# Kernel optimization log

Hardware: AMD Instinct MI355X
Metric: run time of the kernel (lower is better)

The kernel has to match this reference:

```python
import jax, jax.numpy as jnp
import numpy as np

N = 200000      # nodes
E = 1600000     # edges
B = 1000        # graphs
SD = 64         # state_dim
AD = 32         # action_dim
H = 128         # HIDDEN_LAYER
EPS = 1e-5


def setup_inputs() -> dict:
    key = jax.random.key(0)
    ks = jax.random.split(key, 16)
    x = jax.random.normal(ks[0], (N, SD), dtype=jnp.float32)
    action = jax.random.normal(ks[1], (N, AD), dtype=jnp.float32)
    edge_index = jax.random.randint(ks[2], (2, E), 0, N, dtype=jnp.int64)
    batch_size = jnp.sort(jax.random.randint(ks[3], (N,), 0, B, dtype=jnp.int64))
    # parameters (Linear weights stored [in, out]; torch init std=0.1 for fc layers)
    W_gcn = jax.random.normal(ks[4], (SD, H), dtype=jnp.float32) / np.sqrt(SD)
    b_gcn = jnp.zeros((H,), jnp.float32)
    g0 = jnp.ones((H,), jnp.float32); be0 = jnp.zeros((H,), jnp.float32)
    W1 = jax.random.normal(ks[5], (H, H), dtype=jnp.float32) * 0.1
    b1 = jnp.zeros((H,), jnp.float32)
    g1 = jnp.ones((H,), jnp.float32); be1 = jnp.zeros((H,), jnp.float32)
    W2 = jax.random.normal(ks[6], (AD, H), dtype=jnp.float32) * 0.1
    b2 = jnp.zeros((H,), jnp.float32)
    g2 = jnp.ones((H,), jnp.float32); be2 = jnp.zeros((H,), jnp.float32)
    W3 = jax.random.normal(ks[7], (2 * H, 1), dtype=jnp.float32) * 0.1
    b3 = jnp.zeros((1,), jnp.float32)
    return dict(x=x, action=action, W_gcn=W_gcn, b_gcn=b_gcn, g0=g0, be0=be0,
                W1=W1, b1=b1, g1=g1, be1=be1, W2=W2, b2=b2, g2=g2, be2=be2,
                W3=W3, b3=b3, edge_index=edge_index, batch_size=batch_size)


def _bn(h, gamma, beta):
    # BatchNorm1d, training-mode batch statistics over the node axis
    mu = jnp.mean(h, axis=0)
    var = jnp.var(h, axis=0)
    return (h - mu) * jax.lax.rsqrt(var + EPS) * gamma + beta


def _gcn(x, edge_index, W, b):
    # GCN conv with self-loops and symmetric normalization:
    # out_i = sum_{j in N(i) u {i}} (d_i d_j)^{-1/2} (x_j W) + b
    loops = jnp.arange(N, dtype=edge_index.dtype)
    src = jnp.concatenate([edge_index[0], loops])
    dst = jnp.concatenate([edge_index[1], loops])
    deg = jax.ops.segment_sum(jnp.ones_like(dst, dtype=x.dtype), dst, num_segments=N)
    dinv = jax.lax.rsqrt(deg)                       # deg >= 1 due to self-loops
    norm = dinv[src] * dinv[dst]                    # [E+N]
    xw = x @ W                                      # [N, H]
    msg = xw[src] * norm[:, None]                   # [E+N, H]
    return jax.ops.segment_sum(msg, dst, num_segments=N) + b


def reference(x, action, W_gcn, b_gcn, g0, be0, W1, b1, g1, be1,
              W2, b2, g2, be2, W3, b3, edge_index, batch_size):
    h0 = jax.nn.relu(_gcn(x, edge_index, W_gcn, b_gcn))
    h0n = _bn(h0, g0, be0)
    h1 = jax.nn.relu(h0n @ W1 + b1)
    h1n = _bn(h1, g1, be1)
    h2 = jax.nn.relu(action @ W2 + b2)
    h2n = _bn(h2, g2, be2)
    feat = jnp.concatenate([h1n, h2n], axis=1)      # [N, 2H]
    sums = jax.ops.segment_sum(feat, batch_size, num_segments=B)
    cnts = jax.ops.segment_sum(jnp.ones((N,), feat.dtype), batch_size, num_segments=B)
    pooled = sums / jnp.maximum(cnts, 1.0)[:, None]  # [B, 2H]
    return pooled @ W3 + b3                          # [B, 1]
```

## Files before the change

### kernel.cpp

```cpp
#include <hip/hip_runtime.h>

typedef unsigned short u16;
typedef unsigned int   u32;
typedef __bf16 bf16x8 __attribute__((ext_vector_type(8)));
typedef float  f32x4  __attribute__((ext_vector_type(4)));

#define EPS 1e-5f
#define BSHIFT 9

__device__ __forceinline__ float b2f(u16 u){ union{u32 i; float f;} v; v.i=((u32)u)<<16; return v.f; }
__device__ __forceinline__ u16 f2b(float f){
  u32 x = __float_as_uint(f);
  u32 r = x + 0x7fffu + ((x>>16)&1u);
  return (u16)(r>>16);
}

template<int K, bool RELU, bool HASBIAS, bool AF32, bool POOL>
__global__ __launch_bounds__(256) void k_gemm(const void* __restrict__ Av,
                                              const u16* __restrict__ BhiT,
                                              const u16* __restrict__ BloT,
                                              const float* __restrict__ bias,
                                              u16* __restrict__ C,
                                              float* __restrict__ stats,
                                              const int* __restrict__ batch,
                                              float* __restrict__ P, int M)
{
  constexpr int KM = K / 8;
  constexpr int KR = K / 32;
  __shared__ u16 lds[2 * 64 * K];
  __shared__ float sred[64], qred[64];
  const int tid = threadIdx.x;
  const int halfg = gridDim.x >> 1;
  const int ch = (blockIdx.x >= halfg) ? 1 : 0;
  const int t0 = blockIdx.x - ch * halfg;
  for (int i = tid; i < 64 * KM; i += 256) {
    const int n = i / KM, kb = i % KM;
    const int kb2 = kb ^ (n & (KM - 1));
    const int gsrc = ((ch * 64 + n) * KM + kb) * 8;
    *(uint4*)(&lds[(n * KM + kb2) * 8])          = *(const uint4*)(BhiT + gsrc);
    *(uint4*)(&lds[64 * K + (n * KM + kb2) * 8]) = *(const uint4*)(BloT + gsrc);
  }
  if (tid < 64) { sred[tid] = 0.f; qred[tid] = 0.f; }
  __syncthreads();
  const int wid = tid >> 6, lane = tid & 63, q = lane >> 4, r16 = lane & 15;
  const int nmt = (M + 127) >> 7;
  float ls[4], lq[4];
#pragma unroll
  for (int nb = 0; nb < 4; nb++) { ls[nb] = 0.f; lq[nb] = 0.f; }
  float bv[4];
#pragma unroll
  for (int nb = 0; nb < 4; nb++) bv[nb] = HASBIAS ? bias[ch * 64 + nb * 16 + r16] : 0.f;

  for (int mt = t0; mt < nmt; mt += halfg) {
    const int row0 = mt << 7;
    const bool ok1 = (row0 + 64) < M;

    bf16x8 av[2][KR];
    if (AF32) {
      const float* Af = (const float*)Av + (size_t)(row0 + (wid << 4) + r16) * K + q * 8;
#pragma unroll
      for (int kk = 0; kk < KR; kk++) {
        f32x4 x0 = *(const f32x4*)(Af + kk * 32);
        f32x4 x1 = *(const f32x4*)(Af + kk * 32 + 4);
#pragma unroll
        for (int j = 0; j < 4; j++) { av[0][kk][j] = (__bf16)x0[j]; av[0][kk][4 + j] = (__bf16)x1[j]; }
      }
      if (ok1) {
        const float* Ag = Af + (size_t)64 * K;
#pragma unroll
        for (int kk = 0; kk < KR; kk++) {
          f32x4 x0 = *(const f32x4*)(Ag + kk * 32);
          f32x4 x1 = *(const f32x4*)(Ag + kk * 32 + 4);
#pragma unroll
          for (int j = 0; j < 4; j++) { av[1][kk][j] = (__bf16)x0[j]; av[1][kk][4 + j] = (__bf16)x1[j]; }
        }
      }
    } else {
      const u16* Ab = (const u16*)Av + (size_t)(row0 + (wid << 4) + r16) * K + q * 8;
#pragma unroll
      for (int kk = 0; kk < KR; kk++) av[0][kk] = *(const bf16x8*)(Ab + kk * 32);
      if (ok1) {
#pragma unroll
        for (int kk = 0; kk < KR; kk++) av[1][kk] = *(const bf16x8*)(Ab + (size_t)64 * K + kk * 32);
      }
    }

    f32x4 acc[2][4];
#pragma unroll
    for (int rt = 0; rt < 2; rt++)
#pragma unroll
      for (int nb = 0; nb < 4; nb++) acc[rt][nb] = (f32x4){0.f, 0.f, 0.f, 0.f};
#pragma unroll
    for (int kk = 0; kk < KR; kk++) {
#pragma unroll
      for (int nb = 0; nb < 4; nb++) {
        const int n = nb * 16 + r16;
        const int kb2 = (kk * 4 + q) ^ (n & (KM - 1));
        const bf16x8 bh = *(const bf16x8*)(&lds[(n * KM + kb2) * 8]);
        const bf16x8 bl = *(const bf16x8*)(&lds[64 * K + (n * KM + kb2) * 8]);
        acc[0][nb] = __builtin_amdgcn_mfma_f32_16x16x32_bf16(av[0][kk], bh, acc[0][nb], 0, 0, 0);
        acc[0][nb] = __builtin_amdgcn_mfma_f32_16x16x32_bf16(av[0][kk], bl, acc[0][nb], 0, 0, 0);
        if (ok1) {
          acc[1][nb] = __builtin_amdgcn_mfma_f32_16x16x32_bf16(av[1][kk], bh, acc[1][nb], 0, 0, 0);
          acc[1][nb] = __builtin_amdgcn_mfma_f32_16x16x32_bf16(av[1][kk], bl, acc[1][nb], 0, 0, 0);
        }
      }
    }

#pragma unroll
    for (int rt = 0; rt < 2; rt++) {
      if (rt && !ok1) continue;
      const int rbase = row0 + rt * 64 + (wid << 4) + (q << 2);
#pragma unroll
      for (int nb = 0; nb < 4; nb++) {
        const int col = ch * 64 + nb * 16 + r16;
#pragma unroll
        for (int r = 0; r < 4; r++) {
          float v = acc[rt][nb][r] + bv[nb];
          if (RELU) v = fmaxf(v, 0.f);
          ls[nb] += v; lq[nb] += v * v;
          if (!POOL) C[(size_t)(rbase + r) * 128 + col] = f2b(v);
          else acc[rt][nb][r] = v;
        }
      }
      if (POOL) {
        int bg[4];
#pragma unroll
        for (int r = 0; r < 4; r++) bg[r] = batch[rbase + r];
        const int g0 = __shfl(bg[0], 0, 64);
        const int g1 = __shfl(bg[3], 48, 64);
        for (int g = g0; g <= g1; ++g) {
#pragma unroll
          for (int nb = 0; nb < 4; nb++) {
            float sv = 0.f;
#pragma unroll
            for (int r = 0; r < 4; r++) sv += (bg[r] == g) ? acc[rt][nb][r] : 0.f;
            sv += __shfl_xor(sv, 16, 64);
            sv += __shfl_xor(sv, 32, 64);
            if (q == 0) atomicAdd(&P[g * 128 + ch * 64 + nb * 16 + r16], sv);
          }
        }
      }
    }
  }
#pragma unroll
  for (int nb = 0; nb < 4; nb++) {
    atomicAdd(&sred[nb * 16 + r16], ls[nb]);
    atomicAdd(&qred[nb * 16 + r16], lq[nb]);
  }
  __syncthreads();
  if (tid < 64) {
    atomicAdd(&stats[ch * 64 + tid], sred[tid]);
    atomicAdd(&stats[128 + ch * 64 + tid], qred[tid]);
  }
}

__global__ void k_prep0(const float* __restrict__ Wg, const float* __restrict__ W2,
                        u16* __restrict__ WghiT, u16* __restrict__ WgloT,
                        u16* __restrict__ W2hiT, u16* __restrict__ W2loT,
                        const int* __restrict__ batch, int* __restrict__ gofs,
                        int* __restrict__ zbase, int zwords, int NZ, int N, int B)
{
  const int bid = blockIdx.x, t = threadIdx.x;
  if (bid < NZ) {
    const int i = bid * 2048 + t * 8;
    if (i < zwords) {
      *(int4*)(zbase + i)     = make_int4(0, 0, 0, 0);
      *(int4*)(zbase + i + 4) = make_int4(0, 0, 0, 0);
    }
  } else if (bid < NZ + 48) {
    const int i = (bid - NZ) * 256 + t;
    if (i < 64 * 128) {
      int k = i >> 7, n = i & 127;
      float w = Wg[i]; u16 h = f2b(w);
      WghiT[n * 64 + k] = h; WgloT[n * 64 + k] = f2b(w - b2f(h));
    } else if (i < 64 * 128 + 32 * 128) {
      int j = i - 64 * 128;
      int k = j >> 7, n = j & 127;
      float w = W2[j]; u16 h = f2b(w);
      W2hiT[n * 32 + k] = h; W2loT[n * 32 + k] = f2b(w - b2f(h));
    }
  } else {
    const int i = (bid - NZ - 48) * 256 + t;
    if (i == 0) { for (int g = 0; g <= batch[0]; g++) gofs[g] = 0; }
    if (i == N - 1) { for (int g = batch[N - 1] + 1; g <= B; g++) gofs[g] = N; }
    if (i < N - 1) {
      const int b0 = batch[i], b1 = batch[i + 1];
      for (int g = b0 + 1; g <= b1; g++) gofs[g] = i + 1;
    }
  }
}

__global__ __launch_bounds__(256) void k_bincnt(const int* __restrict__ dst, int* __restrict__ btot,
                                                int E, int NB)
{
  extern __shared__ int hist[];
  const int tid = threadIdx.x;
  for (int i = tid; i < NB; i += 256) hist[i] = 0;
  __syncthreads();
  const int chunk = (E + gridDim.x - 1) / gridDim.x;
  const int start = blockIdx.x * chunk;
  const int end = min(start + chunk, E);
  for (int e = start + tid; e < end; e += 256) atomicAdd(&hist[((u32)dst[e]) >> BSHIFT], 1);
  __syncthreads();
  for (int i = tid; i < NB; i += 256) if (hist[i]) atomicAdd(&btot[i], hist[i]);
}

__global__ void k_exscan(const int* __restrict__ in, int* __restrict__ out, int n)
{
  __shared__ int s[256];
  const int t = threadIdx.x;
  const int per = (n + 255) / 256;
  const int base = t * per;
  int loc[8]; int sum = 0;
  for (int j = 0; j < per; j++) { int v = (base + j < n) ? in[base + j] : 0; loc[j] = sum; sum += v; }
  s[t] = sum; __syncthreads();
  for (int o = 1; o < 256; o <<= 1) {
    int x = (t >= o) ? s[t - o] : 0;
    __syncthreads();
    s[t] += x;
    __syncthreads();
  }
  const int ex = s[t] - sum;
  for (int j = 0; j < per; j++) if (base + j < n) out[base + j] = ex + loc[j];
  if (t == 255) out[n] = s[255];
}

__global__ __launch_bounds__(256) void k_bin(const int* __restrict__ src, const int* __restrict__ dst,
                                             const int* __restrict__ bbase, int* __restrict__ bcur,
                                             uint2* __restrict__ pairs, int E, int NB)
{
  extern __shared__ int lds[];
  int* hist = lds; int* wbase = lds + NB;
  const int tid = threadIdx.x;
  for (int i = tid; i < NB; i += 256) hist[i] = 0;
  __syncthreads();
  const int chunk = (E + gridDim.x - 1) / gridDim.x;
  const int start = blockIdx.x * chunk;
  const int end = min(start + chunk, E);
  for (int e = start + tid; e < end; e += 256) atomicAdd(&hist[((u32)dst[e]) >> BSHIFT], 1);
  __syncthreads();
  for (int i = tid; i < NB; i += 256) {
    int c = hist[i];
    wbase[i] = c ? bbase[i] + atomicAdd(&bcur[i], c) : 0;
    hist[i] = 0;
  }
  __syncthreads();
  for (int e = start + tid; e < end; e += 256) {
    const int d = dst[e];
    const int b = ((u32)d) >> BSHIFT;
    const int o = atomicAdd(&hist[b], 1);
    pairs[wbase[b] + o] = make_uint2((u32)d, (u32)src[e]);
  }
}

__global__ __launch_bounds__(256) void k_bucket(const uint2* __restrict__ pairs,
                                                const int* __restrict__ bbase,
                                                const float* __restrict__ x,
                                                int* __restrict__ offsets, float* __restrict__ dinv,
                                                int* __restrict__ elist, u16* __restrict__ y,
                                                int N, int NB, int Etot)
{
  __shared__ int hist[512];
  __shared__ int scan[256];
  __shared__ int lcur[512];
  __shared__ float sdinv[512];
  const int b = blockIdx.x, t = threadIdx.x;
  const int nbase = b << BSHIFT;
  const int nn = min(1 << BSHIFT, N - nbase);
  hist[t] = 0; hist[256 + t] = 0;
  __syncthreads();
  const int p0 = bbase[b], p1 = bbase[b + 1];
  for (int p = p0 + t; p < p1; p += 256) atomicAdd(&hist[pairs[p].x - nbase], 1);
  __syncthreads();
  const int h0 = hist[2 * t], h1 = hist[2 * t + 1];
  const int psum = h0 + h1;
  scan[t] = psum; __syncthreads();
  for (int o = 1; o < 256; o <<= 1) {
    int xx = (t >= o) ? scan[t - o] : 0;
    __syncthreads();
    scan[t] += xx;
    __syncthreads();
  }
  const int ex = scan[t] - psum;
  const int li0 = 2 * t, li1 = 2 * t + 1;
  if (li0 < nn) {
    const int i = nbase + li0;
    const int off = p0 + ex + i;
    const float d = rsqrtf((float)(h0 + 1));
    offsets[i] = off; elist[off] = i; lcur[li0] = off + 1;
    dinv[i] = d; sdinv[li0] = d;
  }
  if (li1 < nn) {
    const int i = nbase + li1;
    const int off = p0 + ex + h0 + i;
    const float d = rsqrtf((float)(h1 + 1));
    offsets[i] = off; elist[off] = i; lcur[li1] = off + 1;
    dinv[i] = d; sdinv[li1] = d;
  }
  if (b == NB - 1 && t == 0) offsets[N] = Etot;
  __syncthreads();
  for (int p = p0 + t; p < p1; p += 256) {
    const uint2 pr = pairs[p];
    const int pos = atomicAdd(&lcur[pr.x - nbase], 1);
    elist[pos] = (int)pr.y;
  }
  const size_t ebase = (size_t)nbase * 64;
  const int total = nn * 64;
  for (int i = t * 8; i < total; i += 256 * 8) {
    const float d = sdinv[i >> 6];
    f32x4 a = *(const f32x4*)(x + ebase + i);
    f32x4 c = *(const f32x4*)(x + ebase + i + 4);
    u16 o[8];
#pragma unroll
    for (int j = 0; j < 4; j++) { o[j] = f2b(a[j] * d); o[4 + j] = f2b(c[j] * d); }
    *(uint4*)(y + ebase + i) = *(uint4*)o;
  }
}

__global__ __launch_bounds__(256) void k_agg(const u16* __restrict__ y, const int* __restrict__ offsets,
                                             const int* __restrict__ elist, const float* __restrict__ dinv,
                                             u16* __restrict__ aggx, int n)
{
  const int lane = threadIdx.x & 63;
  const int half = lane >> 5, l32 = lane & 31;
  const int g4 = l32 >> 3, sub = lane & 7;
  const int wid  = (blockIdx.x * 256 + threadIdx.x) >> 6;
  const int nw   = gridDim.x * 4;
  const int npair = (n + 1) >> 1;
  for (int pr = wid; pr < npair; pr += nw) {
    const int node = pr * 2 + half;
    const int s0 = offsets[node], s1 = offsets[node + 1];
    const int mydeg = s1 - s0;
    const int degA = __shfl(mydeg, 0, 64);
    const int degB = __shfl(mydeg, 32, 64);
    const int degmax = max(degA, degB);
    float a[8];
#pragma unroll
    for (int t = 0; t < 8; t++) a[t] = 0.f;
    for (int base = 0; base < degmax; base += 32) {
      const int m = mydeg - base;
      const int ev = (base + l32 < mydeg) ? elist[s0 + base + l32] : 0;
      const int iters = (min(32, degmax - base) + 3) >> 2;
      for (int it = 0; it < iters; it++) {
        const int j = it * 4 + g4;
        const int idx = __shfl(ev, half * 32 + j, 64);
        if (j < m) {
          const uint4 v = *(const uint4*)(y + (size_t)idx * 64 + sub * 8);
          const u32 w[4] = {v.x, v.y, v.z, v.w};
#pragma unroll
          for (int t = 0; t < 4; t++) {
            a[2 * t]     += b2f((u16)w[t]);
            a[2 * t + 1] += b2f((u16)(w[t] >> 16));
          }
        }
      }
    }
#pragma unroll
    for (int t = 0; t < 8; t++) {
      a[t] += __shfl_xor(a[t], 8, 64);
      a[t] += __shfl_xor(a[t], 16, 64);
    }
    if (g4 == 0) {
      const float di = dinv[node];
      u16 o[8];
#pragma unroll
      for (int t = 0; t < 8; t++) o[t] = f2b(a[t] * di);
      *(uint4*)(aggx + (size_t)node * 64 + sub * 8) = *(uint4*)o;
    }
  }
}

__global__ void k_prep1(const float* __restrict__ stats0, const float* __restrict__ W1,
                        const float* __restrict__ b1, const float* __restrict__ g0,
                        const float* __restrict__ be0, u16* __restrict__ W1hiT,
                        u16* __restrict__ W1loT, float* __restrict__ b1p, float n)
{
  __shared__ float A[8], Csh[8];
  const int t = threadIdx.x;
  if (t < 8) {
    const int k = blockIdx.x * 8 + t;
    const float mu = stats0[k] / n;
    const float var = fmaxf(stats0[128 + k] / n - mu * mu, 0.f);
    const float a = g0[k] * rsqrtf(var + EPS);
    A[t] = a; Csh[t] = be0[k] - mu * a;
  }
  __syncthreads();
  float acc = (blockIdx.x == 0) ? b1[t] : 0.f;
#pragma unroll
  for (int kk = 0; kk < 8; kk++) {
    const int k = blockIdx.x * 8 + kk;
    const float w0 = W1[k * 128 + t];
    acc += Csh[kk] * w0;
    const float w = A[kk] * w0;
    const u16 h = f2b(w);
    W1hiT[t * 128 + k] = h;
    W1loT[t * 128 + k] = f2b(w - b2f(h));
  }
  atomicAdd(&b1p[t], acc);
}

__global__ void k_prep2(const float* __restrict__ stats1, const float* __restrict__ stats2,
                        const float* __restrict__ g1, const float* __restrict__ be1,
                        const float* __restrict__ g2, const float* __restrict__ be2,
                        const float* __restrict__ W3, const float* __restrict__ b3,
                        float* __restrict__ w1f, float* __restrict__ w2f,
                        float* __restrict__ constS, float n)
{
  __shared__ float red[256];
  const int t = threadIdx.x;
  float c, wv;
  if (t < 128) {
    const float mu = stats1[t] / n;
    const float var = fmaxf(stats1[128 + t] / n - mu * mu, 0.f);
    const float a = g1[t] * rsqrtf(var + EPS);
    c = be1[t] - mu * a;
    wv = W3[t];
    w1f[t] = a * wv;
  } else {
    const int f = t - 128;
    const float mu = stats2[f] / n;
    const float var = fmaxf(stats2[128 + f] / n - mu * mu, 0.f);
    const float a = g2[f] * rsqrtf(var + EPS);
    c = be2[f] - mu * a;
    wv = W3[t];
    w2f[f] = a * wv;
  }
  red[t] = c * wv; __syncthreads();
  for (int o = 128; o; o >>= 1) { if (t < o) red[t] += red[t + o]; __syncthreads(); }
  if (t == 0) { constS[0] = red[0] + b3[0]; constS[1] = b3[0]; }
}

__global__ void k_out2(const float* __restrict__ P1, const float* __restrict__ P2,
                       const int* __restrict__ gofs, const float* __restrict__ w1f,
                       const float* __restrict__ w2f, const float* __restrict__ constS,
                       float* __restrict__ out, int B)
{
  const int lane = threadIdx.x & 63;
  const int g = (blockIdx.x * 256 + threadIdx.x) >> 6;
  if (g >= B) return;
  const int c = gofs[g + 1] - gofs[g];
  const int k = 2 * lane;
  float d = P1[g * 128 + k] * w1f[k] + P1[g * 128 + k + 1] * w1f[k + 1]
          + P2[g * 128 + k] * w2f[k] + P2[g * 128 + k + 1] * w2f[k + 1];
#pragma unroll
  for (int o = 1; o < 64; o <<= 1) d += __shfl_xor(d, o, 64);
  if (lane == 0) out[g] = (c > 0) ? d / (float)c + constS[0] : constS[1];
}

extern "C" void kernel_launch(void* const* d_in, const int* in_sizes, int n_in,
                              void* d_out, int out_size, void* d_ws, size_t ws_size,
                              hipStream_t stream)
{
  const float* x    = (const float*)d_in[0];
  const float* act  = (const float*)d_in[1];
  const float* Wg   = (const float*)d_in[2];
  const float* bg   = (const float*)d_in[3];
  const float* g0   = (const float*)d_in[4];
  const float* be0  = (const float*)d_in[5];
  const float* W1   = (const float*)d_in[6];
  const float* b1   = (const float*)d_in[7];
  const float* g1   = (const float*)d_in[8];
  const float* be1  = (const float*)d_in[9];
  const float* W2   = (const float*)d_in[10];
  const float* b2   = (const float*)d_in[11];
  const float* g2   = (const float*)d_in[12];
  const float* be2  = (const float*)d_in[13];
  const float* W3   = (const float*)d_in[14];
  const float* b3   = (const float*)d_in[15];
  const int* eidx   = (const int*)d_in[16];
  const int* batch  = (const int*)d_in[17];

  const int N = in_sizes[17];
  const int E = in_sizes[16] / 2;
  const int B = out_size;
  const int* src = eidx;
  const int* dst = eidx + E;
  const int NB = (N + (1 << BSHIFT) - 1) >> BSHIFT;

  char* ws = (char*)d_ws;
  size_t off = 0;
  auto alloc = [&](size_t bytes) -> char* {
    off = (off + 255) & ~(size_t)255;
    char* p = ws + off; off += bytes; return p;
  };

  u16* bufA = (u16*)alloc((size_t)N * 128 * 2);
  u16* xb   = (u16*)alloc((size_t)N * 64 * 2);
  u16* aggx = (u16*)alloc((size_t)N * 64 * 2);

  int zwords = 768 + 128 + 2 * NB + 2 * 128 * B;
  zwords = (zwords + 7) & ~7;
  char* zbase   = alloc((size_t)zwords * 4);
  float* stats0 = (float*)zbase;
  float* stats1 = stats0 + 256;
  float* stats2 = stats1 + 256;
  float* b1p    = stats2 + 256;
  int*   btot   = (int*)(b1p + 128);
  int*   bcur   = btot + NB;
  float* P1     = (float*)(bcur + NB);
  float* P2     = P1 + 128 * B;

  int*   offsets = (int*)alloc((size_t)(N + 1) * 4);
  float* dinv    = (float*)alloc((size_t)N * 4);
  int*   elist   = (int*)alloc((size_t)(E + N) * 4);
  uint2* pairs   = (uint2*)alloc((size_t)E * 8);
  int*   bbase   = (int*)alloc((size_t)(NB + 1) * 4);
  int*   gofs    = (int*)alloc((size_t)(B + 1) * 4);
  u16*   WghiT   = (u16*)alloc(128 * 64 * 2);
  u16*   WgloT   = (u16*)alloc(128 * 64 * 2);
  u16*   W1hiT   = (u16*)alloc(128 * 128 * 2);
  u16*   W1loT   = (u16*)alloc(128 * 128 * 2);
  u16*   W2hiT   = (u16*)alloc(128 * 32 * 2);
  u16*   W2loT   = (u16*)alloc(128 * 32 * 2);
  float* w1f     = (float*)alloc(128 * 4);
  float* w2f     = (float*)alloc(128 * 4);
  float* constS  = (float*)alloc(2 * 4);

  u16* h0 = bufA;

  const int NZ = (zwords + 2047) / 2048;
  const int nbounds = (N + 255) / 256;
  k_prep0<<<NZ + 48 + nbounds, 256, 0, stream>>>(Wg, W2, WghiT, WgloT, W2hiT, W2loT,
                                                 batch, gofs, (int*)zbase, zwords, NZ, N, B);
  k_bincnt<<<256, 256, NB * 4, stream>>>(dst, btot, E, NB);
  k_exscan<<<1, 256, 0, stream>>>(btot, bbase, NB);
  k_bin<<<256, 256, 2 * NB * 4, stream>>>(src, dst, bbase, bcur, pairs, E, NB);
  k_bucket<<<NB, 256, 0, stream>>>(pairs, bbase, x, offsets, dinv, elist, xb, N, NB, E + N);
  k_agg<<<2048, 256, 0, stream>>>(xb, offsets, elist, dinv, aggx, N);
  k_gemm<64, true, true, false, false><<<768, 256, 0, stream>>>(aggx, WghiT, WgloT, bg,
                                                                h0, stats0, nullptr, nullptr, N);
  k_prep1<<<16, 128, 0, stream>>>(stats0, W1, b1, g0, be0, W1hiT, W1loT, b1p, (float)N);
  k_gemm<128, true, true, false, true><<<768, 256, 0, stream>>>(h0, W1hiT, W1loT, b1p,
                                                                nullptr, stats1, batch, P1, N);
  k_gemm<32, true, true, true, true><<<768, 256, 0, stream>>>(act, W2hiT, W2loT, b2,
                                                              nullptr, stats2, batch, P2, N);
  k_prep2<<<1, 256, 0, stream>>>(stats1, stats2, g1, be1, g2, be2, W3, b3, w1f, w2f, constS, (float)N);
  k_out2<<<(B * 64 + 255) / 256, 256, 0, stream>>>(P1, P2, gofs, w1f, w2f, constS, (float*)d_out, B);
}
```

Baseline: 376.5 us.

## Assign contiguous row tiles per block and coalesce pooling atomics across tiles

Each GEMM block now handles a contiguous range of 128-row tiles instead of a strided set. The pooling step merges both 64-row halves per tile before reducing, and keeps a running per-graph partial sum across consecutive tiles. It issues one atomicAdd per lane only when the graph id changes. Grid size rises from 768 to 1024 blocks. The aim is to cut global atomic traffic to the pooled buffer, in exchange for more per-graph loop iterations over a wider graph range.

```diff
diff --git a/kernel.cpp b/kernel.cpp
--- a/kernel.cpp
+++ b/kernel.cpp
@@ -44,6 +44,9 @@
   __syncthreads();
   const int wid = tid >> 6, lane = tid & 63, q = lane >> 4, r16 = lane & 15;
   const int nmt = (M + 127) >> 7;
+  const int qt = nmt / halfg, rm = nmt % halfg;
+  const int tstart = (t0 < rm) ? t0 * (qt + 1) : rm * (qt + 1) + (t0 - rm) * qt;
+  const int tend   = tstart + ((t0 < rm) ? qt + 1 : qt);
   float ls[4], lq[4];
 #pragma unroll
   for (int nb = 0; nb < 4; nb++) { ls[nb] = 0.f; lq[nb] = 0.f; }
@@ -51,7 +54,10 @@
 #pragma unroll
   for (int nb = 0; nb < 4; nb++) bv[nb] = HASBIAS ? bias[ch * 64 + nb * 16 + r16] : 0.f;
 
-  for (int mt = t0; mt < nmt; mt += halfg) {
+  int gc = -1;
+  float rs = 0.f;
+
+  for (int mt = tstart; mt < tend; mt++) {
     const int row0 = mt << 7;
     const bool ok1 = (row0 + 64) < M;
 
@@ -123,26 +129,47 @@
           else acc[rt][nb][r] = v;
         }
       }
-      if (POOL) {
-        int bg[4];
-#pragma unroll
-        for (int r = 0; r < 4; r++) bg[r] = batch[rbase + r];
-        const int g0 = __shfl(bg[0], 0, 64);
-        const int g1 = __shfl(bg[3], 48, 64);
-        for (int g = g0; g <= g1; ++g) {
-#pragma unroll
-          for (int nb = 0; nb < 4; nb++) {
-            float sv = 0.f;
-#pragma unroll
-            for (int r = 0; r < 4; r++) sv += (bg[r] == g) ? acc[rt][nb][r] : 0.f;
-            sv += __shfl_xor(sv, 16, 64);
-            sv += __shfl_xor(sv, 32, 64);
-            if (q == 0) atomicAdd(&P[g * 128 + ch * 64 + nb * 16 + r16], sv);
+    }
+
+    if (POOL) {
+      int bg0[4], bg1[4];
+      const int rb0 = row0 + (wid << 4) + (q << 2);
+#pragma unroll
+      for (int r = 0; r < 4; r++) bg0[r] = batch[rb0 + r];
+      if (ok1) {
+#pragma unroll
+        for (int r = 0; r < 4; r++) bg1[r] = batch[rb0 + 64 + r];
+      } else {
+#pragma unroll
+        for (int r = 0; r < 4; r++) bg1[r] = bg0[r];
+      }
+      const int gA = __shfl(bg0[0], 0, 64);
+      const int gB = ok1 ? __shfl(bg1[3], 48, 64) : __shfl(bg0[3], 48, 64);
+      for (int g = gA; g <= gB; ++g) {
+        float cs = 0.f;
+#pragma unroll
+        for (int nb = 0; nb < 4; nb++) {
+          float sv = 0.f;
+#pragma unroll
+          for (int r = 0; r < 4; r++) sv += (bg0[r] == g) ? acc[0][nb][r] : 0.f;
+          if (ok1) {
+#pragma unroll
+            for (int r = 0; r < 4; r++) sv += (bg1[r] == g) ? acc[1][nb][r] : 0.f;
           }
+          sv += __shfl_xor(sv, 16, 64);
+          sv += __shfl_xor(sv, 32, 64);
+          cs = (q == nb) ? sv : cs;
         }
-      }
-    }
-  }
+        if (g == gc) {
+          rs += cs;
+        } else {
+          if (gc >= 0) atomicAdd(&P[gc * 128 + ch * 64 + lane], rs);
+          gc = g; rs = cs;
+        }
+      }
+    }
+  }
+  if (POOL && gc >= 0) atomicAdd(&P[gc * 128 + ch * 64 + lane], rs);
 #pragma unroll
   for (int nb = 0; nb < 4; nb++) {
     atomicAdd(&sred[nb * 16 + r16], ls[nb]);
@@ -528,13 +555,13 @@
   k_bin<<<256, 256, 2 * NB * 4, stream>>>(src, dst, bbase, bcur, pairs, E, NB);
   k_bucket<<<NB, 256, 0, stream>>>(pairs, bbase, x, offsets, dinv, elist, xb, N, NB, E + N);
   k_agg<<<2048, 256, 0, stream>>>(xb, offsets, elist, dinv, aggx, N);
-  k_gemm<64, true, true, false, false><<<768, 256, 0, stream>>>(aggx, WghiT, WgloT, bg,
-                                                                h0, stats0, nullptr, nullptr, N);
+  k_gemm<64, true, true, false, false><<<1024, 256, 0, stream>>>(aggx, WghiT, WgloT, bg,
+                                                                 h0, stats0, nullptr, nullptr, N);
   k_prep1<<<16, 128, 0, stream>>>(stats0, W1, b1, g0, be0, W1hiT, W1loT, b1p, (float)N);
-  k_gemm<128, true, true, false, true><<<768, 256, 0, stream>>>(h0, W1hiT, W1loT, b1p,
-                                                                nullptr, stats1, batch, P1, N);
-  k_gemm<32, true, true, true, true><<<768, 256, 0, stream>>>(act, W2hiT, W2loT, b2,
-                                                              nullptr, stats2, batch, P2, N);
+  k_gemm<128, true, true, false, true><<<1024, 256, 0, stream>>>(h0, W1hiT, W1loT, b1p,
+                                                                 nullptr, stats1, batch, P1, N);
+  k_gemm<32, true, true, true, true><<<1024, 256, 0, stream>>>(act, W2hiT, W2loT, b2,
+                                                               nullptr, stats2, batch, P2, N);
   k_prep2<<<1, 256, 0, stream>>>(stats1, stats2, g1, be1, g2, be2, W3, b3, w1f, w2f, constS, (float)N);
   k_out2<<<(B * 64 + 255) / 256, 256, 0, stream>>>(P1, P2, gofs, w1f, w2f, constS, (float*)d_out, B);
 }
```

Result: slower. 400.7 us (+6.4%).
